# Kernel tuning notes

Measured on AMD Instinct MI355X. Metric: run time of the kernel, lower is better.

The kernel has to match this reference:

```python
import jax, jax.numpy as jnp
import numpy as np

IN_C = 31
OUT_C = 31
GRID = 5          # grid_size
K = 3             # spline_order
NUM_BASIS = GRID + K                  # 8 B-spline basis functions
COEF_LEN = IN_C * OUT_C * NUM_BASIS   # 7688
UW_LEN = IN_C * OUT_C                 # 961 (univariate_weight)
RW_LEN = IN_C * OUT_C                 # 961 (residual_weight)
PNUM = COEF_LEN + UW_LEN + RW_LEN     # 9610 = kan_params_num


def _ext_grid():
    # uniform grid on grid_range=(-1,1), extended by K knots on each side
    h = 2.0 / GRID
    return jnp.arange(-K, GRID + K + 1, dtype=jnp.float32) * h - 1.0  # (GRID+2K+1,)


def bspline_basis(x):
    # x: (N, IN_C) -> (N, IN_C, NUM_BASIS) via Cox-de Boor recursion
    grid = _ext_grid()
    xx = x[..., None]
    b = ((xx >= grid[:-1]) & (xx < grid[1:])).astype(x.dtype)
    for p in range(1, K + 1):
        left = (xx - grid[: -(p + 1)]) / (grid[p:-1] - grid[: -(p + 1)]) * b[..., :-1]
        right = (grid[p + 1:] - xx) / (grid[p + 1:] - grid[1:-p]) * b[..., 1:]
        b = left + right
    return b


def setup_inputs() -> dict:
    key = jax.random.key(0)
    k1, k2, k3 = jax.random.split(key, 3)
    x = jax.random.normal(k1, (1, IN_C, 128, 128), jnp.float32)
    # HyperspectralGeneratorLayer: per-pixel (1x1 conv) map in_channels -> kan_params_num
    gen_w = jax.random.normal(k2, (PNUM, IN_C), jnp.float32) * 0.02
    gen_b = jax.random.normal(k3, (PNUM,), jnp.float32) * 0.02
    return {"x": x, "gen_w": gen_w, "gen_b": gen_b}


def reference(x, gen_w, gen_b):
    B, C, H, W = x.shape
    xf = x.transpose(0, 2, 3, 1).reshape(B * H * W, C)      # (N, 31)
    # generator: per-pixel KAN parameter vector (N, 9610)
    w = xf @ gen_w.T + gen_b
    coef = w[:, :COEF_LEN].reshape(-1, IN_C, OUT_C, NUM_BASIS)
    uw = w[:, COEF_LEN:COEF_LEN + UW_LEN].reshape(-1, IN_C, OUT_C)
    rw = w[:, COEF_LEN + UW_LEN:].reshape(-1, IN_C, OUT_C)
    # per-pixel KAN: phi_ij(x_i) = uw_ij * spline_ij(x_i) + rw_ij * silu(x_i); y_j = sum_i phi_ij
    basis = bspline_basis(xf)                               # (N, 31, 8)
    spline = jnp.einsum('nik,niok->nio', basis, coef)       # (N, 31, 31)
    y = jnp.einsum('nio,nio->no', spline, uw) \
        + jnp.einsum('ni,nio->no', jax.nn.silu(xf), rw)     # (N, 31)
    return y.reshape(B, H, W, OUT_C).transpose(0, 3, 1, 2)
```

## Files before the change

kernel.cpp:

```cpp
#include <hip/hip_runtime.h>
#include <hip/hip_bf16.h>
#include <math.h>

#define IN_C 31
#define OUT_C 31
#define NPIX 16384
#define UW_OFF 7688
#define RW_OFF 8649
#define PART_OFF (640 * 1024)
#define CHUNK_BYTES 20480

typedef __attribute__((ext_vector_type(8))) short bf16x8;
typedef __attribute__((ext_vector_type(4))) float f32x4;

__device__ inline short f2bf(float f) {
    union { __hip_bfloat16 h; short s; } cv;
    cv.h = __float2bfloat16(f);
    return cv.s;
}

__global__ __launch_bounds__(64) void kan_prep_kernel(
    const float* __restrict__ gw, const float* __restrict__ gb,
    unsigned short* __restrict__ ws)
{
    const int blk = blockIdx.x;
    const int i   = blk / 20;
    const int ch  = blk % 20;
    const int l   = threadIdx.x;
    const int col = l & 15;
    const int krow = l >> 4;
    const int o = (ch & 1) * 16 + col;

    int p;
    if (ch < 16)      p = (i * 31 + o) * 8 + (ch >> 1);
    else if (ch < 18) p = UW_OFF + i * 31 + o;
    else              p = RW_OFF + i * 31 + o;

    bf16x8 v8;
#pragma unroll
    for (int j = 0; j < 8; ++j) {
        const int c = krow * 8 + j;
        float v = 0.f;
        if (o < OUT_C) v = (c < IN_C) ? gw[p * 31 + c] : gb[p];
        v8[j] = f2bf(v);
    }
    ((bf16x8*)ws)[blk * 64 + l] = v8;
}

__device__ __forceinline__ void stage_i(const unsigned char* wsrc,
                                        unsigned char* ldst, int t) {
#pragma unroll
    for (int k = 0; k < 5; ++k) {
        const int off = (k * 256 + t) * 16;
        __builtin_amdgcn_global_load_lds(
            (const __attribute__((address_space(1))) unsigned int*)(wsrc + off),
            (__attribute__((address_space(3))) unsigned int*)(ldst + off),
            16, 0, 0);
    }
}

__global__ __launch_bounds__(256, 4) void kan_mfma5_kernel(
    const float* __restrict__ x,
    const unsigned char* __restrict__ wsw,
    float* __restrict__ parts,
    float* __restrict__ out,
    int nsplit)
{
    const int t = threadIdx.x;
    const int l = t & 63;
    const int w = t >> 6;
    const int pix0 = blockIdx.x * 128;
    const int csize = (IN_C + nsplit - 1) / nsplit;
    const int ibase = blockIdx.y * csize;
    const int ni = min(csize, IN_C - ibase);

    __shared__ __align__(16) unsigned char wlds[CHUNK_BYTES];

    const int n0 = w * 32;

    float xf[2][8];
    bf16x8 ax[2];
#pragma unroll
    for (int mt = 0; mt < 2; ++mt) {
        const int row = pix0 + n0 + mt * 16 + (l & 15);
        const int cb = (l >> 4) * 8;
#pragma unroll
        for (int j = 0; j < 8; ++j) {
            const int c = cb + j;
            xf[mt][j] = (c < IN_C) ? x[c * NPIX + row] : 1.0f;
        }
#pragma unroll
        for (int j = 0; j < 8; ++j) ax[mt][j] = f2bf(xf[mt][j]);
    }

    f32x4 Y[2][2];
#pragma unroll
    for (int mt = 0; mt < 2; ++mt)
#pragma unroll
        for (int nt = 0; nt < 2; ++nt) Y[mt][nt] = (f32x4){0.f, 0.f, 0.f, 0.f};

#pragma unroll 1
    for (int tt_i = 0; tt_i < ni; ++tt_i) {
        const int i = ibase + tt_i;

        stage_i(wsw + (size_t)i * CHUNK_BYTES, wlds, t);

        float bas[2][8];
        bf16x8 arw[2];
#pragma unroll
        for (int mt = 0; mt < 2; ++mt) {
            const float xv = x[i * NPIX + pix0 + n0 + mt * 16 + (l & 15)];
            const float tb = (xv + 2.2f) * 2.5f;
            const float jf = floorf(tb);
            const float u  = tb - jf;
            const int  jj  = (int)jf;
            const float u2 = u * u, u3 = u2 * u;
            const float b0v = u3 * (1.f / 6.f);
            const float b1v = (-3.f * u3 + 3.f * u2 + 3.f * u + 1.f) * (1.f / 6.f);
            const float b2v = (3.f * u3 - 6.f * u2 + 4.f) * (1.f / 6.f);
            const float omu = 1.f - u;
            const float b3v = omu * omu * omu * (1.f / 6.f);
#pragma unroll
            for (int m = 0; m < 8; ++m) {
                const int d = jj - m;
                bas[mt][m] = (d == 0) ? b0v : (d == 1) ? b1v : (d == 2) ? b2v
                           : (d == 3) ? b3v : 0.f;
            }
            const float sil = xv / (1.f + __expf(-xv));
#pragma unroll
            for (int j = 0; j < 8; ++j) arw[mt][j] = f2bf(sil * xf[mt][j]);
        }

        __syncthreads();

        const unsigned char* wb = wlds;

        f32x4 SP[2][2], UW[2][2];
#pragma unroll
        for (int mt = 0; mt < 2; ++mt)
#pragma unroll
            for (int nt = 0; nt < 2; ++nt) {
                SP[mt][nt] = (f32x4){0.f, 0.f, 0.f, 0.f};
                UW[mt][nt] = (f32x4){0.f, 0.f, 0.f, 0.f};
            }

#pragma unroll
        for (int kc = 0; kc < 8; ++kc) {
            const bf16x8 b0 = *(const bf16x8*)(wb + ((kc * 2 + 0) * 64 + l) * 16);
            const bf16x8 b1 = *(const bf16x8*)(wb + ((kc * 2 + 1) * 64 + l) * 16);
#pragma unroll
            for (int mt = 0; mt < 2; ++mt) {
                bf16x8 af;
#pragma unroll
                for (int j = 0; j < 8; ++j) af[j] = f2bf(bas[mt][kc] * xf[mt][j]);
                SP[mt][0] = __builtin_amdgcn_mfma_f32_16x16x32_bf16(af, b0, SP[mt][0], 0, 0, 0);
                SP[mt][1] = __builtin_amdgcn_mfma_f32_16x16x32_bf16(af, b1, SP[mt][1], 0, 0, 0);
            }
        }
        {
            const bf16x8 u0 = *(const bf16x8*)(wb + (16 * 64 + l) * 16);
            const bf16x8 u1 = *(const bf16x8*)(wb + (17 * 64 + l) * 16);
#pragma unroll
            for (int mt = 0; mt < 2; ++mt) {
                UW[mt][0] = __builtin_amdgcn_mfma_f32_16x16x32_bf16(ax[mt], u0, UW[mt][0], 0, 0, 0);
                UW[mt][1] = __builtin_amdgcn_mfma_f32_16x16x32_bf16(ax[mt], u1, UW[mt][1], 0, 0, 0);
            }
        }
        {
            const bf16x8 r0 = *(const bf16x8*)(wb + (18 * 64 + l) * 16);
            const bf16x8 r1 = *(const bf16x8*)(wb + (19 * 64 + l) * 16);
#pragma unroll
            for (int mt = 0; mt < 2; ++mt) {
                Y[mt][0] = __builtin_amdgcn_mfma_f32_16x16x32_bf16(arw[mt], r0, Y[mt][0], 0, 0, 0);
                Y[mt][1] = __builtin_amdgcn_mfma_f32_16x16x32_bf16(arw[mt], r1, Y[mt][1], 0, 0, 0);
            }
        }
#pragma unroll
        for (int mt = 0; mt < 2; ++mt)
#pragma unroll
            for (int nt = 0; nt < 2; ++nt)
#pragma unroll
                for (int r = 0; r < 4; ++r)
                    Y[mt][nt][r] += UW[mt][nt][r] * SP[mt][nt][r];

        __syncthreads();
    }

    float* yb = (float*)wlds;
#pragma unroll
    for (int mt = 0; mt < 2; ++mt)
#pragma unroll
        for (int nt = 0; nt < 2; ++nt)
#pragma unroll
            for (int r = 0; r < 4; ++r) {
                const int p = n0 + mt * 16 + (l >> 4) * 4 + r;
                const int o = nt * 16 + (l & 15);
                if (o < OUT_C) yb[p * 33 + o] = Y[mt][nt][r];
            }
    __syncthreads();

    float* dst = (blockIdx.y == 0) ? out
               : (parts + (size_t)(blockIdx.y - 1) * OUT_C * NPIX);
    for (int idx = t; idx < 128 * OUT_C; idx += 256) {
        const int n = idx & 127, o = idx >> 7;
        dst[o * NPIX + pix0 + n] = yb[n * 33 + o];
    }
}

__global__ __launch_bounds__(256) void kan_combine_kernel(
    float* __restrict__ out, const float* __restrict__ parts, int npart)
{
    const int e = blockIdx.x * 256 + threadIdx.x;
    const int nv = (OUT_C * NPIX) / 4;
    if (e < nv) {
        f32x4 a = ((const f32x4*)out)[e];
        for (int j = 0; j < npart; ++j)
            a += ((const f32x4*)parts)[e + (size_t)j * nv];
        ((f32x4*)out)[e] = a;
    }
}

extern "C" void kernel_launch(void* const* d_in, const int* in_sizes, int n_in,
                              void* d_out, int out_size, void* d_ws, size_t ws_size,
                              hipStream_t stream) {
    const float* x  = (const float*)d_in[0];
    const float* gw = (const float*)d_in[1];
    const float* gb = (const float*)d_in[2];
    float* out = (float*)d_out;
    unsigned short* ws = (unsigned short*)d_ws;
    float* parts = (float*)((char*)d_ws + PART_OFF);

    const size_t part_bytes = (size_t)OUT_C * NPIX * 4;
    int nsplit = 16;
    if (ws_size < PART_OFF + 15 * part_bytes) nsplit = 8;
    if (ws_size < PART_OFF + 7 * part_bytes)  nsplit = 4;

    hipLaunchKernelGGL(kan_prep_kernel, dim3(620), dim3(64), 0, stream, gw, gb, ws);
    hipLaunchKernelGGL(kan_mfma5_kernel, dim3(NPIX / 128, nsplit), dim3(256), 0, stream,
                       x, (const unsigned char*)d_ws, parts, out, nsplit);
    const int nv = (OUT_C * NPIX) / 4;
    hipLaunchKernelGGL(kan_combine_kernel, dim3((nv + 255) / 256), dim3(256), 0, stream,
                       out, parts, nsplit - 1);
}
```

Measured before the change: 47.74 us.

## Swap MFMA operands and apply basis weight after MFMA instead of per-element conversion

The spline MFMA now uses the weights as the A operand and the unmodified bf16 input vector as B, producing a transposed output tile (outputs on rows, pixels on columns). Each lane then scales the MFMA result by its pixel's scalar basis value with FMAs, instead of building a fresh bf16 operand (basis times x, eight conversions) for every basis index. This removes most of the per-iteration float-to-bf16 conversion work, but each MFMA starts from a zero accumulator and needs extra VALU FMAs to accumulate. The launch-bounds occupancy hint is also dropped and the epilogue indexing is adjusted to match the transposed layout.

```diff
diff --git a/kernel.cpp b/kernel.cpp
--- a/kernel.cpp
+++ b/kernel.cpp
@@ -59,7 +59,7 @@
     }
 }
 
-__global__ __launch_bounds__(256, 4) void kan_mfma5_kernel(
+__global__ __launch_bounds__(256) void kan_mfma6_kernel(
     const float* __restrict__ x,
     const unsigned char* __restrict__ wsw,
     float* __restrict__ parts,
@@ -81,23 +81,25 @@
     float xf[2][8];
     bf16x8 ax[2];
 #pragma unroll
-    for (int mt = 0; mt < 2; ++mt) {
-        const int row = pix0 + n0 + mt * 16 + (l & 15);
+    for (int pt = 0; pt < 2; ++pt) {
+        const int row = pix0 + n0 + pt * 16 + (l & 15);
         const int cb = (l >> 4) * 8;
 #pragma unroll
         for (int j = 0; j < 8; ++j) {
             const int c = cb + j;
-            xf[mt][j] = (c < IN_C) ? x[c * NPIX + row] : 1.0f;
-        }
-#pragma unroll
-        for (int j = 0; j < 8; ++j) ax[mt][j] = f2bf(xf[mt][j]);
+            xf[pt][j] = (c < IN_C) ? x[c * NPIX + row] : 1.0f;
+        }
+#pragma unroll
+        for (int j = 0; j < 8; ++j) ax[pt][j] = f2bf(xf[pt][j]);
     }
 
     f32x4 Y[2][2];
 #pragma unroll
-    for (int mt = 0; mt < 2; ++mt)
-#pragma unroll
-        for (int nt = 0; nt < 2; ++nt) Y[mt][nt] = (f32x4){0.f, 0.f, 0.f, 0.f};
+    for (int ot = 0; ot < 2; ++ot)
+#pragma unroll
+        for (int pt = 0; pt < 2; ++pt) Y[ot][pt] = (f32x4){0.f, 0.f, 0.f, 0.f};
+
+    const f32x4 zero4 = (f32x4){0.f, 0.f, 0.f, 0.f};
 
 #pragma unroll 1
     for (int tt_i = 0; tt_i < ni; ++tt_i) {
@@ -108,8 +110,8 @@
         float bas[2][8];
         bf16x8 arw[2];
 #pragma unroll
-        for (int mt = 0; mt < 2; ++mt) {
-            const float xv = x[i * NPIX + pix0 + n0 + mt * 16 + (l & 15)];
+        for (int pt = 0; pt < 2; ++pt) {
+            const float xv = x[i * NPIX + pix0 + n0 + pt * 16 + (l & 15)];
             const float tb = (xv + 2.2f) * 2.5f;
             const float jf = floorf(tb);
             const float u  = tb - jf;
@@ -123,79 +125,80 @@
 #pragma unroll
             for (int m = 0; m < 8; ++m) {
                 const int d = jj - m;
-                bas[mt][m] = (d == 0) ? b0v : (d == 1) ? b1v : (d == 2) ? b2v
+                bas[pt][m] = (d == 0) ? b0v : (d == 1) ? b1v : (d == 2) ? b2v
                            : (d == 3) ? b3v : 0.f;
             }
             const float sil = xv / (1.f + __expf(-xv));
 #pragma unroll
-            for (int j = 0; j < 8; ++j) arw[mt][j] = f2bf(sil * xf[mt][j]);
+            for (int j = 0; j < 8; ++j) arw[pt][j] = f2bf(sil * xf[pt][j]);
         }
 
         __syncthreads();
 
         const unsigned char* wb = wlds;
 
-        f32x4 SP[2][2], UW[2][2];
-#pragma unroll
-        for (int mt = 0; mt < 2; ++mt)
-#pragma unroll
-            for (int nt = 0; nt < 2; ++nt) {
-                SP[mt][nt] = (f32x4){0.f, 0.f, 0.f, 0.f};
-                UW[mt][nt] = (f32x4){0.f, 0.f, 0.f, 0.f};
-            }
-
-#pragma unroll
-        for (int kc = 0; kc < 8; ++kc) {
-            const bf16x8 b0 = *(const bf16x8*)(wb + ((kc * 2 + 0) * 64 + l) * 16);
-            const bf16x8 b1 = *(const bf16x8*)(wb + ((kc * 2 + 1) * 64 + l) * 16);
-#pragma unroll
-            for (int mt = 0; mt < 2; ++mt) {
-                bf16x8 af;
-#pragma unroll
-                for (int j = 0; j < 8; ++j) af[j] = f2bf(bas[mt][kc] * xf[mt][j]);
-                SP[mt][0] = __builtin_amdgcn_mfma_f32_16x16x32_bf16(af, b0, SP[mt][0], 0, 0, 0);
-                SP[mt][1] = __builtin_amdgcn_mfma_f32_16x16x32_bf16(af, b1, SP[mt][1], 0, 0, 0);
-            }
-        }
+        f32x4 SP[2][2];
+#pragma unroll
+        for (int ot = 0; ot < 2; ++ot)
+#pragma unroll
+            for (int pt = 0; pt < 2; ++pt) SP[ot][pt] = zero4;
+
+#pragma unroll
+        for (int k = 0; k < 8; ++k) {
+            const bf16x8 a0 = *(const bf16x8*)(wb + ((k * 2 + 0) * 64 + l) * 16);
+            const bf16x8 a1 = *(const bf16x8*)(wb + ((k * 2 + 1) * 64 + l) * 16);
+#pragma unroll
+            for (int pt = 0; pt < 2; ++pt) {
+                const f32x4 T0 = __builtin_amdgcn_mfma_f32_16x16x32_bf16(a0, ax[pt], zero4, 0, 0, 0);
+                const f32x4 T1 = __builtin_amdgcn_mfma_f32_16x16x32_bf16(a1, ax[pt], zero4, 0, 0, 0);
+                const float bk = bas[pt][k];
+#pragma unroll
+                for (int r = 0; r < 4; ++r) {
+                    SP[0][pt][r] = fmaf(bk, T0[r], SP[0][pt][r]);
+                    SP[1][pt][r] = fmaf(bk, T1[r], SP[1][pt][r]);
+                }
+            }
+        }
+        f32x4 UW[2][2];
         {
             const bf16x8 u0 = *(const bf16x8*)(wb + (16 * 64 + l) * 16);
             const bf16x8 u1 = *(const bf16x8*)(wb + (17 * 64 + l) * 16);
 #pragma unroll
-            for (int mt = 0; mt < 2; ++mt) {
-                UW[mt][0] = __builtin_amdgcn_mfma_f32_16x16x32_bf16(ax[mt], u0, UW[mt][0], 0, 0, 0);
-                UW[mt][1] = __builtin_amdgcn_mfma_f32_16x16x32_bf16(ax[mt], u1, UW[mt][1], 0, 0, 0);
+            for (int pt = 0; pt < 2; ++pt) {
+                UW[0][pt] = __builtin_amdgcn_mfma_f32_16x16x32_bf16(u0, ax[pt], zero4, 0, 0, 0);
+                UW[1][pt] = __builtin_amdgcn_mfma_f32_16x16x32_bf16(u1, ax[pt], zero4, 0, 0, 0);
             }
         }
         {
             const bf16x8 r0 = *(const bf16x8*)(wb + (18 * 64 + l) * 16);
             const bf16x8 r1 = *(const bf16x8*)(wb + (19 * 64 + l) * 16);
 #pragma unroll
-            for (int mt = 0; mt < 2; ++mt) {
-                Y[mt][0] = __builtin_amdgcn_mfma_f32_16x16x32_bf16(arw[mt], r0, Y[mt][0], 0, 0, 0);
-                Y[mt][1] = __builtin_amdgcn_mfma_f32_16x16x32_bf16(arw[mt], r1, Y[mt][1], 0, 0, 0);
-            }
-        }
-#pragma unroll
-        for (int mt = 0; mt < 2; ++mt)
-#pragma unroll
-            for (int nt = 0; nt < 2; ++nt)
+            for (int pt = 0; pt < 2; ++pt) {
+                Y[0][pt] = __builtin_amdgcn_mfma_f32_16x16x32_bf16(r0, arw[pt], Y[0][pt], 0, 0, 0);
+                Y[1][pt] = __builtin_amdgcn_mfma_f32_16x16x32_bf16(r1, arw[pt], Y[1][pt], 0, 0, 0);
+            }
+        }
+#pragma unroll
+        for (int ot = 0; ot < 2; ++ot)
+#pragma unroll
+            for (int pt = 0; pt < 2; ++pt)
 #pragma unroll
                 for (int r = 0; r < 4; ++r)
-                    Y[mt][nt][r] += UW[mt][nt][r] * SP[mt][nt][r];
+                    Y[ot][pt][r] = fmaf(UW[ot][pt][r], SP[ot][pt][r], Y[ot][pt][r]);
 
         __syncthreads();
     }
 
     float* yb = (float*)wlds;
 #pragma unroll
-    for (int mt = 0; mt < 2; ++mt)
-#pragma unroll
-        for (int nt = 0; nt < 2; ++nt)
+    for (int ot = 0; ot < 2; ++ot)
+#pragma unroll
+        for (int pt = 0; pt < 2; ++pt)
 #pragma unroll
             for (int r = 0; r < 4; ++r) {
-                const int p = n0 + mt * 16 + (l >> 4) * 4 + r;
-                const int o = nt * 16 + (l & 15);
-                if (o < OUT_C) yb[p * 33 + o] = Y[mt][nt][r];
+                const int o = ot * 16 + (l >> 4) * 4 + r;
+                const int p = n0 + pt * 16 + (l & 15);
+                if (o < OUT_C) yb[p * 33 + o] = Y[ot][pt][r];
             }
     __syncthreads();
 
@@ -236,7 +239,7 @@
     if (ws_size < PART_OFF + 7 * part_bytes)  nsplit = 4;
 
     hipLaunchKernelGGL(kan_prep_kernel, dim3(620), dim3(64), 0, stream, gw, gb, ws);
-    hipLaunchKernelGGL(kan_mfma5_kernel, dim3(NPIX / 128, nsplit), dim3(256), 0, stream,
+    hipLaunchKernelGGL(kan_mfma6_kernel, dim3(NPIX / 128, nsplit), dim3(256), 0, stream,
                        x, (const unsigned char*)d_ws, parts, out, nsplit);
     const int nv = (OUT_C * NPIX) / 4;
     hipLaunchKernelGGL(kan_combine_kernel, dim3((nv + 255) / 256), dim3(256), 0, stream,
```

After: 58.97 us. +23.5%, slower.
